# Performance work log

Hardware: AMD Instinct MI355X
Metric: run time of the kernel (lower is better)

Reference implementation:

```python
import jax, jax.numpy as jnp
import numpy as np

N_NODES = 100000
N_EDGES = 1600000
D_IN = 128
D_HID = 128
D_OUT = 32


def setup_inputs() -> dict:
    key = jax.random.key(0)
    ks = jax.random.split(key, 10)
    x = jax.random.normal(ks[0], (N_NODES, D_IN), dtype=jnp.float32)
    edge_index = jax.random.randint(ks[1], (2, N_EDGES), 0, N_NODES, dtype=jnp.int64)
    s = 0.05
    return {
        "x": x,
        "edge_index": edge_index,
        "Wl0": jax.random.normal(ks[2], (D_IN, D_HID), jnp.float32) * s,
        "bl0": jnp.zeros((D_HID,), jnp.float32),
        "Wr0": jax.random.normal(ks[3], (D_IN, D_HID), jnp.float32) * s,
        "Wl1": jax.random.normal(ks[4], (D_HID, D_HID), jnp.float32) * s,
        "bl1": jnp.zeros((D_HID,), jnp.float32),
        "Wr1": jax.random.normal(ks[5], (D_HID, D_HID), jnp.float32) * s,
        "Wl2": jax.random.normal(ks[6], (D_HID, D_OUT), jnp.float32) * s,
        "bl2": jnp.zeros((D_OUT,), jnp.float32),
        "Wr2": jax.random.normal(ks[7], (D_HID, D_OUT), jnp.float32) * s,
    }


def _sage_conv(x, src, dst, Wl, bl, Wr):
    # PyG SAGEConv (aggr='mean', root_weight=True):
    # out[i] = lin_l(mean_{j in N(i)} x_j) + lin_r(x_i)
    n = x.shape[0]
    msgs = x[src]                                        # [E, F] gather
    agg = jax.ops.segment_sum(msgs, dst, num_segments=n) # [N, F] scatter-add
    deg = jax.ops.segment_sum(jnp.ones((src.shape[0],), x.dtype), dst, num_segments=n)
    mean = agg / jnp.maximum(deg, 1.0)[:, None]
    return mean @ Wl + bl + x @ Wr


def reference(x, edge_index, Wl0, bl0, Wr0, Wl1, bl1, Wr1, Wl2, bl2, Wr2):
    src, dst = edge_index[0], edge_index[1]
    h = jax.nn.relu(_sage_conv(x, src, dst, Wl0, bl0, Wr0))
    h = jax.nn.relu(_sage_conv(h, src, dst, Wl1, bl1, Wr1))
    h = _sage_conv(h, src, dst, Wl2, bl2, Wr2)
    return jax.nn.log_softmax(h, axis=1)
```

## Files before the change

kernel.cpp:

```cpp
#include <hip/hip_runtime.h>
#include <hip/hip_bf16.h>
#include <math.h>

#define NN 100000
#define NE 1600000

#define NCB 391
#define EB  2048
#define SCT 512
#define EPT 4
#define HBK 128
#define NSB 782
#define WPB 144
#define NGB 782

typedef __attribute__((ext_vector_type(8))) short short8;
typedef __attribute__((ext_vector_type(4))) float f32x4;
typedef __attribute__((ext_vector_type(2))) float f32x2;

__device__ __forceinline__ unsigned short f2bf(float f) {
  union { float f; unsigned int i; } v; v.f = f;
  unsigned int i = v.i;
  unsigned int r = (i + 0x7FFFu + ((i >> 16) & 1u)) >> 16;
  return (unsigned short)r;
}
__device__ __forceinline__ float bflo(unsigned int u) {
  union { unsigned int i; float f; } v; v.i = u << 16; return v.f;
}
__device__ __forceinline__ float bfhi(unsigned int u) {
  union { unsigned int i; float f; } v; v.i = u & 0xFFFF0000u; return v.f;
}
__device__ __forceinline__ f32x2 up2(unsigned int u) {
  union { unsigned int i; float f; } lo, hi;
  lo.i = u << 16; hi.i = u & 0xFFFF0000u;
  return (f32x2){lo.f, hi.f};
}

__global__ __launch_bounds__(512) void k_prep(
    const int* __restrict__ dst, int* __restrict__ part,
    const float* __restrict__ Wl0, const float* __restrict__ Wr0,
    const float* __restrict__ Wl1, const float* __restrict__ Wr1,
    const float* __restrict__ Wl2, const float* __restrict__ Wr2,
    unsigned short* __restrict__ B0, unsigned short* __restrict__ B1,
    unsigned short* __restrict__ B2) {
  if (blockIdx.x < HBK) {
    __shared__ int h[NCB];
    for (int i = threadIdx.x; i < NCB; i += 512) h[i] = 0;
    __syncthreads();
    int stride = HBK * 512;
    for (int e = blockIdx.x * 512 + threadIdx.x; e < NE; e += stride) {
      int d = dst[e];
      d = d < 0 ? 0 : (d >= NN ? NN - 1 : d);
      atomicAdd(&h[d >> 8], 1);
    }
    __syncthreads();
    for (int i = threadIdx.x; i < NCB; i += 512) part[blockIdx.x * NCB + i] = h[i];
  } else {
    int idx = (blockIdx.x - HBK) * 512 + threadIdx.x;
    if (idx < 32768) {
      int n = idx >> 7, k = idx & 127;
      float v = (n < 128) ? Wl0[k * 128 + n] : Wr0[k * 128 + (n - 128)];
      B0[idx] = f2bf(v);
    } else if (idx < 65536) {
      int j = idx - 32768;
      int n = j >> 7, k = j & 127;
      float v = (n < 128) ? Wl1[k * 128 + n] : Wr1[k * 128 + (n - 128)];
      B1[j] = f2bf(v);
    } else if (idx < 73728) {
      int j = idx - 65536;
      int n = j >> 7, k = j & 127;
      float v = (n < 32) ? Wl2[k * 32 + n] : Wr2[k * 32 + (n - 32)];
      B2[j] = f2bf(v);
    }
  }
}

__global__ __launch_bounds__(512) void k_cscan(const int* __restrict__ part,
                                               int* __restrict__ cboff,
                                               int* __restrict__ ccur,
                                               int* __restrict__ csroff) {
  __shared__ int sd[512];
  int t = threadIdx.x;
  int v = 0;
  if (t < NCB) {
    int s0 = 0, s1 = 0, s2 = 0, s3 = 0;
    #pragma unroll 4
    for (int k = 0; k < HBK; k += 4) {
      s0 += part[(k + 0) * NCB + t];
      s1 += part[(k + 1) * NCB + t];
      s2 += part[(k + 2) * NCB + t];
      s3 += part[(k + 3) * NCB + t];
    }
    v = (s0 + s1) + (s2 + s3);
    ccur[t * 16] = 0;
  }
  sd[t] = v;
  __syncthreads();
  for (int st = 1; st < 512; st <<= 1) {
    int x = (t >= st) ? sd[t - st] : 0;
    __syncthreads();
    sd[t] += x;
    __syncthreads();
  }
  if (t < NCB) cboff[t] = sd[t] - v;
  if (t == NCB - 1) { cboff[NCB] = sd[t]; csroff[NN] = sd[t]; }
}


__device__ __forceinline__ void cscatter_body(
    char* smem, int bid,
    const int* __restrict__ src, const int* __restrict__ dst,
    const int* __restrict__ cboff, int* __restrict__ ccur,
    unsigned int* __restrict__ ebuf) {
  int* lh = (int*)smem;
  int t = threadIdx.x;
  int base = bid * EB;
  for (int i = t; i < NCB; i += SCT) lh[i] = 0;
  __syncthreads();
  unsigned int rk[EPT], pv[EPT];
  #pragma unroll
  for (int i = 0; i < EPT; i++) {
    int e = base + i * SCT + t;
    rk[i] = 0xFFFFFFFFu;
    pv[i] = 0;
    if (e < NE) {
      int d = dst[e];
      d = d < 0 ? 0 : (d >= NN ? NN - 1 : d);
      int s = src[e];
      s = s < 0 ? 0 : (s >= NN ? NN - 1 : s);
      int cb = d >> 8;
      int r = atomicAdd(&lh[cb], 1);
      rk[i] = (((unsigned int)cb) << 13) | (unsigned int)r;
      pv[i] = (((unsigned int)(d & 255)) << 17) | (unsigned int)s;
    }
  }
  __syncthreads();
  for (int i = t; i < NCB; i += SCT) {
    int c = lh[i];
    int g = c ? atomicAdd(&ccur[i * 16], c) : 0;
    lh[i] = cboff[i] + g;
  }
  __syncthreads();
  #pragma unroll
  for (int i = 0; i < EPT; i++) {
    unsigned int r = rk[i];
    if (r != 0xFFFFFFFFu) {
      ebuf[lh[r >> 13] + (r & 0x1FFF)] = pv[i];
    }
  }
}

__device__ __forceinline__ void epilogue256(
    unsigned short* sA, int tid, int nb, int wn, int mbase, int nbase,
    int l15, int lq, f32x4 acc[4][4], const float* __restrict__ bias,
    unsigned short* __restrict__ yl, unsigned short* __restrict__ yr) {
  __syncthreads();
  if (wn < 2) {
    #pragma unroll
    for (int mi = 0; mi < 4; mi++)
      #pragma unroll
      for (int ni = 0; ni < 4; ni++) {
        int n = nbase + ni * 16 + l15;
        #pragma unroll
        for (int r = 0; r < 4; r++)
          sA[(mbase + mi * 16 + lq * 4 + r) * 136 + n] = f2bf(acc[mi][ni][r]);
      }
  }
  __syncthreads();
  {
    int row = tid >> 2, c0 = (tid & 3) * 32;
    int gn = nb + row;
    if (gn < NN) {
      #pragma unroll
      for (int k = 0; k < 4; k++) {
        uint4 v = *(uint4*)&sA[row * 136 + c0 + k * 8];
        *(uint4*)&yl[(size_t)gn * 128 + c0 + k * 8] = v;
      }
    }
  }
  __syncthreads();
  if (wn >= 2) {
    #pragma unroll
    for (int mi = 0; mi < 4; mi++)
      #pragma unroll
      for (int ni = 0; ni < 4; ni++) {
        int n2 = nbase - 128 + ni * 16 + l15;
        float b = bias[n2];
        #pragma unroll
        for (int r = 0; r < 4; r++)
          sA[(mbase + mi * 16 + lq * 4 + r) * 136 + n2] =
              f2bf(acc[mi][ni][r] + b);
      }
  }
  __syncthreads();
  {
    int row = tid >> 2, c0 = (tid & 3) * 32;
    int gn = nb + row;
    if (gn < NN) {
      #pragma unroll
      for (int k = 0; k < 4; k++) {
        uint4 v = *(uint4*)&sA[row * 136 + c0 + k * 8];
        *(uint4*)&yr[(size_t)gn * 128 + c0 + k * 8] = v;
      }
    }
  }
}

__device__ __forceinline__ void mgemm0_body(
    char* smem, int bid, const float* __restrict__ A,
    const unsigned short* __restrict__ Bp, const float* __restrict__ bias,
    unsigned short* __restrict__ yl, unsigned short* __restrict__ yr) {
  unsigned short* sA = (unsigned short*)smem;
  int tid = threadIdx.x;
  int nb  = bid * 128;

  #pragma unroll
  for (int i = 0; i < 8; i++) {
    int j = i * 512 + tid;
    int m = j >> 5;
    int k4 = (j & 31) * 4;
    int gn = nb + m;
    float4 v = make_float4(0.f, 0.f, 0.f, 0.f);
    if (gn < NN) v = *(const float4*)&A[gn * 128 + k4];
    unsigned int p0 = (unsigned int)f2bf(v.x) | ((unsigned int)f2bf(v.y) << 16);
    unsigned int p1 = (unsigned int)f2bf(v.z) | ((unsigned int)f2bf(v.w) << 16);
    *(uint2*)&sA[m * 136 + k4] = make_uint2(p0, p1);
  }
  __syncthreads();

  int wave = tid >> 6, lane = tid & 63;
  int l15 = lane & 15, lq = lane >> 4;
  int wm = wave & 1, wn = wave >> 1;
  int mbase = wm * 64;
  int nbase = wn * 64;

  f32x4 acc[4][4];
  #pragma unroll
  for (int mi = 0; mi < 4; mi++)
    #pragma unroll
    for (int ni = 0; ni < 4; ni++) acc[mi][ni] = (f32x4){0.f, 0.f, 0.f, 0.f};

  #pragma unroll
  for (int kc = 0; kc < 4; kc++) {
    int k0 = kc * 32 + lq * 8;
    short8 af[4], bfr[4];
    #pragma unroll
    for (int ni = 0; ni < 4; ni++)
      bfr[ni] = *(const short8*)&Bp[(nbase + ni * 16 + l15) * 128 + k0];
    #pragma unroll
    for (int mi = 0; mi < 4; mi++)
      af[mi] = *(const short8*)&sA[(mbase + mi * 16 + l15) * 136 + k0];
    #pragma unroll
    for (int mi = 0; mi < 4; mi++)
      #pragma unroll
      for (int ni = 0; ni < 4; ni++)
        acc[mi][ni] = __builtin_amdgcn_mfma_f32_16x16x32_bf16(
            af[mi], bfr[ni], acc[mi][ni], 0, 0, 0);
  }

  epilogue256(sA, tid, nb, wn, mbase, nbase, l15, lq, acc, bias, yl, yr);
}

__global__ __launch_bounds__(512, 4) void k_scatgemm(
    const int* __restrict__ src, const int* __restrict__ dst,
    const int* __restrict__ cboff, int* __restrict__ ccur,
    unsigned int* __restrict__ ebuf,
    const float* __restrict__ x, const unsigned short* __restrict__ B0,
    const float* __restrict__ bias,
    unsigned short* __restrict__ yl, unsigned short* __restrict__ yr) {
  __shared__ char smem[128 * 136 * 2];
  int bid = blockIdx.x;
  if ((bid & 1) == 0) {
    cscatter_body(smem, bid >> 1, src, dst, cboff, ccur, ebuf);
  } else {
    mgemm0_body(smem, bid >> 1, x, B0, bias, yl, yr);
  }
}

__global__ __launch_bounds__(512) void k_crefine(
    const unsigned int* __restrict__ ebuf, const int* __restrict__ cboff,
    int* __restrict__ csroff, float* __restrict__ invd,
    int* __restrict__ csrsrc) {
  __shared__ int lh[256], pos[256], cur[256];
  int b = blockIdx.x, t = threadIdx.x;
  if (t < 256) { lh[t] = 0; cur[t] = 0; }
  __syncthreads();
  int beg = cboff[b], end = cboff[b + 1];
  for (int i = beg + t; i < end; i += 512) atomicAdd(&lh[ebuf[i] >> 17], 1);
  __syncthreads();
  int v = 0;
  if (t < 256) { v = lh[t]; pos[t] = v; }
  __syncthreads();
  for (int st = 1; st < 256; st <<= 1) {
    int x = (t < 256 && t >= st) ? pos[t - st] : 0;
    __syncthreads();
    if (t < 256) pos[t] += x;
    __syncthreads();
  }
  if (t < 256) {
    int nid = b * 256 + t;
    int mybase = cboff[b] + pos[t] - v;
    if (nid < NN) {
      csroff[nid] = mybase;
      invd[nid] = 1.0f / (float)(v < 1 ? 1 : v);
    }
    pos[t] = mybase;
  }
  __syncthreads();
  for (int i = beg + t; i < end; i += 512) {
    unsigned int u = ebuf[i];
    int local = u >> 17;
    int r = atomicAdd(&cur[local], 1);
    csrsrc[pos[local] + r] = (int)(u & 0x1FFFFu);
  }
}

template <int NC>
__global__ __launch_bounds__(512) void k_mgemm(
    const unsigned short* __restrict__ A, const unsigned short* __restrict__ Bp,
    const float* __restrict__ bias,
    unsigned short* __restrict__ yl, unsigned short* __restrict__ yr) {
  __shared__ unsigned short sA[128 * 136];
  int tid = threadIdx.x;
  int nb  = blockIdx.x * 128;

  #pragma unroll
  for (int i = 0; i < 4; i++) {
    int j = i * 512 + tid;
    int m = j >> 4;
    int k8 = (j & 15) * 8;
    int gn = nb + m;
    uint4 v = make_uint4(0, 0, 0, 0);
    if (gn < NN) v = *(const uint4*)&A[gn * 128 + k8];
    *(uint4*)&sA[m * 136 + k8] = v;
  }
  __syncthreads();

  int wave = tid >> 6, lane = tid & 63;
  int l15 = lane & 15, lq = lane >> 4;
  constexpr int MT = (NC == 256) ? 4 : 2;
  constexpr int NT = (NC == 256) ? 4 : 2;
  int wm, wn;
  if (NC == 256) { wm = wave & 1; wn = wave >> 1; }
  else           { wm = wave >> 1; wn = wave & 1; }
  int mbase = wm * (MT * 16);
  int nbase = wn * (NT * 16);

  f32x4 acc[MT][NT];
  #pragma unroll
  for (int mi = 0; mi < MT; mi++)
    #pragma unroll
    for (int ni = 0; ni < NT; ni++) acc[mi][ni] = (f32x4){0.f, 0.f, 0.f, 0.f};

  #pragma unroll
  for (int kc = 0; kc < 4; kc++) {
    int k0 = kc * 32 + lq * 8;
    short8 af[MT], bfr[NT];
    #pragma unroll
    for (int ni = 0; ni < NT; ni++)
      bfr[ni] = *(const short8*)&Bp[(nbase + ni * 16 + l15) * 128 + k0];
    #pragma unroll
    for (int mi = 0; mi < MT; mi++)
      af[mi] = *(const short8*)&sA[(mbase + mi * 16 + l15) * 136 + k0];
    #pragma unroll
    for (int mi = 0; mi < MT; mi++)
      #pragma unroll
      for (int ni = 0; ni < NT; ni++)
        acc[mi][ni] = __builtin_amdgcn_mfma_f32_16x16x32_bf16(
            af[mi], bfr[ni], acc[mi][ni], 0, 0, 0);
  }

  if (NC == 256) {
    f32x4 (*a)[4] = (f32x4(*)[4])acc;
    epilogue256(sA, tid, nb, wn, mbase, nbase, l15, lq, a, bias, yl, yr);
  } else {
    __syncthreads();
    #pragma unroll
    for (int mi = 0; mi < MT; mi++)
      #pragma unroll
      for (int ni = 0; ni < NT; ni++) {
        int n = nbase + ni * 16 + l15;
        float b = (n >= 32) ? bias[n - 32] : 0.f;
        #pragma unroll
        for (int r = 0; r < 4; r++)
          sA[(mbase + mi * 16 + lq * 4 + r) * 72 + n] =
              f2bf(acc[mi][ni][r] + b);
      }
    __syncthreads();
    int row = tid >> 2, c0 = (tid & 3) * 16;
    int gn = nb + row;
    if (gn < NN) {
      uint4 v0 = *(uint4*)&sA[row * 72 + c0];
      uint4 v1 = *(uint4*)&sA[row * 72 + c0 + 8];
      if (c0 < 32) {
        *(uint4*)&yl[(size_t)gn * 32 + c0] = v0;
        *(uint4*)&yl[(size_t)gn * 32 + c0 + 8] = v1;
      } else {
        *(uint4*)&yr[(size_t)gn * 32 + (c0 - 32)] = v0;
        *(uint4*)&yr[(size_t)gn * 32 + (c0 - 32) + 8] = v1;
      }
    }
  }
}

#define ACC8(u) do { \
  A01 += up2((u).x); A23 += up2((u).y); \
  A45 += up2((u).z); A67 += up2((u).w); } while (0)

__global__ __launch_bounds__(256) void k_agg128(
    const unsigned short* __restrict__ yl, const unsigned short* __restrict__ yr,
    const int* __restrict__ off, const int* __restrict__ csr,
    const float* __restrict__ invd, unsigned short* __restrict__ out, int relu) {
  int wid  = (blockIdx.x * 256 + threadIdx.x) >> 6;
  int lane = threadIdx.x & 63;
  if (wid >= NN) return;
  int beg = off[wid], end = off[wid + 1];
  int deg = end - beg;
  int q   = lane >> 4;
  int l16 = lane & 15;
  const uint4* ylp = (const uint4*)yl;

  float sc = invd[wid];
  uint4 rv = ((const uint4*)yr)[wid * 16 + l16];

  f32x2 A01 = (f32x2){0.f, 0.f}, A23 = (f32x2){0.f, 0.f};
  f32x2 A45 = (f32x2){0.f, 0.f}, A67 = (f32x2){0.f, 0.f};

  for (int w0 = 0; w0 < deg; w0 += 64) {
    int ei = w0 + lane;
    int sv = (ei < deg) ? csr[beg + ei] : 0;
    int wcnt = deg - w0; if (wcnt > 64) wcnt = 64;
    int full = wcnt >> 2;
    int p = 0;
    for (; p + 4 <= full; p += 4) {
      int b = p * 4 + q;
      int s0 = __shfl(sv, b,      64);
      int s1 = __shfl(sv, b + 4,  64);
      int s2 = __shfl(sv, b + 8,  64);
      int s3 = __shfl(sv, b + 12, 64);
      uint4 u0 = ylp[s0 * 16 + l16];
      uint4 u1 = ylp[s1 * 16 + l16];
      uint4 u2 = ylp[s2 * 16 + l16];
      uint4 u3 = ylp[s3 * 16 + l16];
      ACC8(u0); ACC8(u1); ACC8(u2); ACC8(u3);
    }
    for (; p < full; p++) {
      int s0 = __shfl(sv, p * 4 + q, 64);
      uint4 u0 = ylp[s0 * 16 + l16];
      ACC8(u0);
    }
    int rem = wcnt & 3;
    if (rem && q < rem) {
      int s0 = __shfl(sv, full * 4 + q, 64);
      uint4 u0 = ylp[s0 * 16 + l16];
      ACC8(u0);
    }
  }

  float a0 = A01.x, a1 = A01.y, a2 = A23.x, a3 = A23.y;
  float a4 = A45.x, a5 = A45.y, a6 = A67.x, a7 = A67.y;

  a0 += __shfl_xor(a0, 16, 64); a0 += __shfl_xor(a0, 32, 64);
  a1 += __shfl_xor(a1, 16, 64); a1 += __shfl_xor(a1, 32, 64);
  a2 += __shfl_xor(a2, 16, 64); a2 += __shfl_xor(a2, 32, 64);
  a3 += __shfl_xor(a3, 16, 64); a3 += __shfl_xor(a3, 32, 64);
  a4 += __shfl_xor(a4, 16, 64); a4 += __shfl_xor(a4, 32, 64);
  a5 += __shfl_xor(a5, 16, 64); a5 += __shfl_xor(a5, 32, 64);
  a6 += __shfl_xor(a6, 16, 64); a6 += __shfl_xor(a6, 32, 64);
  a7 += __shfl_xor(a7, 16, 64); a7 += __shfl_xor(a7, 32, 64);

  float v0 = a0 * sc + bflo(rv.x), v1 = a1 * sc + bfhi(rv.x);
  float v2 = a2 * sc + bflo(rv.y), v3 = a3 * sc + bfhi(rv.y);
  float v4 = a4 * sc + bflo(rv.z), v5 = a5 * sc + bfhi(rv.z);
  float v6 = a6 * sc + bflo(rv.w), v7 = a7 * sc + bfhi(rv.w);
  if (relu) {
    v0 = fmaxf(v0, 0.f); v1 = fmaxf(v1, 0.f);
    v2 = fmaxf(v2, 0.f); v3 = fmaxf(v3, 0.f);
    v4 = fmaxf(v4, 0.f); v5 = fmaxf(v5, 0.f);
    v6 = fmaxf(v6, 0.f); v7 = fmaxf(v7, 0.f);
  }
  if (q == 0) {
    unsigned int p0 = (unsigned int)f2bf(v0) | ((unsigned int)f2bf(v1) << 16);
    unsigned int p1 = (unsigned int)f2bf(v2) | ((unsigned int)f2bf(v3) << 16);
    unsigned int p2 = (unsigned int)f2bf(v4) | ((unsigned int)f2bf(v5) << 16);
    unsigned int p3 = (unsigned int)f2bf(v6) | ((unsigned int)f2bf(v7) << 16);
    ((uint4*)out)[wid * 16 + l16] = make_uint4(p0, p1, p2, p3);
  }
}

#define ACC4(u) do { \
  A01 += up2((u).x); A23 += up2((u).y); } while (0)

__global__ __launch_bounds__(256) void k_agg32_lsm(
    const unsigned short* __restrict__ yl, const unsigned short* __restrict__ yr,
    const int* __restrict__ off, const int* __restrict__ csr,
    const float* __restrict__ invd, float* __restrict__ out) {
  int wid  = (blockIdx.x * 256 + threadIdx.x) >> 6;
  int lane = threadIdx.x & 63;
  if (wid >= NN) return;
  int beg = off[wid], end = off[wid + 1];
  int deg = end - beg;
  int q  = lane >> 3;
  int l8 = lane & 7;
  const uint2* ylp = (const uint2*)yl;

  float sc = invd[wid];
  uint2 rv = ((const uint2*)yr)[wid * 8 + l8];

  f32x2 A01 = (f32x2){0.f, 0.f}, A23 = (f32x2){0.f, 0.f};

  for (int w0 = 0; w0 < deg; w0 += 64) {
    int ei = w0 + lane;
    int sv = (ei < deg) ? csr[beg + ei] : 0;
    int wcnt = deg - w0; if (wcnt > 64) wcnt = 64;
    int full = wcnt >> 3;
    int p = 0;
    for (; p + 2 <= full; p += 2) {
      int b = p * 8 + q;
      int s0 = __shfl(sv, b,     64);
      int s1 = __shfl(sv, b + 8, 64);
      uint2 u0 = ylp[s0 * 8 + l8];
      uint2 u1 = ylp[s1 * 8 + l8];
      ACC4(u0); ACC4(u1);
    }
    for (; p < full; p++) {
      int s0 = __shfl(sv, p * 8 + q, 64);
      uint2 u0 = ylp[s0 * 8 + l8];
      ACC4(u0);
    }
    int rem = wcnt & 7;
    if (rem && q < rem) {
      int s0 = __shfl(sv, full * 8 + q, 64);
      uint2 u0 = ylp[s0 * 8 + l8];
      ACC4(u0);
    }
  }

  float a0 = A01.x, a1 = A01.y, a2 = A23.x, a3 = A23.y;

  a0 += __shfl_xor(a0, 8, 64); a0 += __shfl_xor(a0, 16, 64); a0 += __shfl_xor(a0, 32, 64);
  a1 += __shfl_xor(a1, 8, 64); a1 += __shfl_xor(a1, 16, 64); a1 += __shfl_xor(a1, 32, 64);
  a2 += __shfl_xor(a2, 8, 64); a2 += __shfl_xor(a2, 16, 64); a2 += __shfl_xor(a2, 32, 64);
  a3 += __shfl_xor(a3, 8, 64); a3 += __shfl_xor(a3, 16, 64); a3 += __shfl_xor(a3, 32, 64);

  float v0 = a0 * sc + bflo(rv.x), v1 = a1 * sc + bfhi(rv.x);
  float v2 = a2 * sc + bflo(rv.y), v3 = a3 * sc + bfhi(rv.y);

  float m = fmaxf(fmaxf(v0, v1), fmaxf(v2, v3));
  m = fmaxf(m, __shfl_xor(m, 1, 64));
  m = fmaxf(m, __shfl_xor(m, 2, 64));
  m = fmaxf(m, __shfl_xor(m, 4, 64));
  float e0 = expf(v0 - m), e1 = expf(v1 - m);
  float e2 = expf(v2 - m), e3 = expf(v3 - m);
  float s = (e0 + e1) + (e2 + e3);
  s += __shfl_xor(s, 1, 64);
  s += __shfl_xor(s, 2, 64);
  s += __shfl_xor(s, 4, 64);
  float ls = logf(s);
  if (q == 0) {
    float4 o = make_float4(v0 - m - ls, v1 - m - ls, v2 - m - ls, v3 - m - ls);
    ((float4*)out)[wid * 8 + l8] = o;
  }
}


extern "C" void kernel_launch(void* const* d_in, const int* in_sizes, int n_in,
                              void* d_out, int out_size, void* d_ws, size_t ws_size,
                              hipStream_t stream) {
  (void)in_sizes; (void)n_in; (void)out_size; (void)ws_size;
  const float* x   = (const float*)d_in[0];
  const int*   ei  = (const int*)d_in[1];
  const float* Wl0 = (const float*)d_in[2];
  const float* bl0 = (const float*)d_in[3];
  const float* Wr0 = (const float*)d_in[4];
  const float* Wl1 = (const float*)d_in[5];
  const float* bl1 = (const float*)d_in[6];
  const float* Wr1 = (const float*)d_in[7];
  const float* Wl2 = (const float*)d_in[8];
  const float* bl2 = (const float*)d_in[9];
  const float* Wr2 = (const float*)d_in[10];
  const int* srcI = ei;
  const int* dstI = ei + NE;

  char* w = (char*)d_ws;
  int*   cboff  = (int*)(w + (32 << 10));
  unsigned short* B0 = (unsigned short*)(w + (64 << 10));
  unsigned short* B1 = (unsigned short*)(w + (160 << 10));
  unsigned short* B2 = (unsigned short*)(w + (256 << 10));
  int*   part   = (int*)(w + (288 << 10));
  int*   ccur   = (int*)(w + (496 << 10));
  int*   csroff = (int*)(w + (1024 << 10));
  float* invd   = (float*)(w + (1536 << 10));
  unsigned int* ebuf = (unsigned int*)(w + (size_t)(2) * 1024 * 1024);
  int*   csrsrc = (int*)(w + (size_t)(9) * 1024 * 1024);
  unsigned short* ylb = (unsigned short*)(w + (size_t)(16) * 1024 * 1024);
  unsigned short* yrb = (unsigned short*)(w + (size_t)(48) * 1024 * 1024);
  unsigned short* hb  = (unsigned short*)(w + (size_t)(80) * 1024 * 1024);

  dim3 gg(NGB);

  k_prep<<<HBK + WPB, 512, 0, stream>>>(dstI, part, Wl0, Wr0, Wl1, Wr1, Wl2, Wr2,
                                        B0, B1, B2);
  k_cscan<<<1, 512, 0, stream>>>(part, cboff, ccur, csroff);
  k_scatgemm<<<NSB + NGB, 512, 0, stream>>>(srcI, dstI, cboff, ccur, ebuf,
                                            x, B0, bl0, ylb, yrb);
  k_crefine<<<NCB, 512, 0, stream>>>(ebuf, cboff, csroff, invd, csrsrc);
  k_agg128<<<(NN * 64) / 256, 256, 0, stream>>>(ylb, yrb, csroff, csrsrc, invd, hb, 1);
  k_mgemm<256><<<gg, 512, 0, stream>>>(hb, B1, bl1, ylb, yrb);
  k_agg128<<<(NN * 64) / 256, 256, 0, stream>>>(ylb, yrb, csroff, csrsrc, invd, hb, 1);
  k_mgemm<64><<<gg, 512, 0, stream>>>(hb, B2, bl2, ylb, yrb);
  k_agg32_lsm<<<(NN * 64) / 256, 256, 0, stream>>>(ylb, yrb, csroff, csrsrc, invd,
                                                   (float*)d_out);
}
```

Baseline: 414.5 us.

## Overlap second-half aggregation with first-half GEMM in fused kernels

Splits each hidden layer's aggregation into two node halves. The first half runs alone. A fused kernel then interleaves GEMM blocks for the first half with aggregation waves for the second half, and a final GEMM launch covers the remaining rows. Layer outputs go to separate yl buffers so the fused kernel never overwrites inputs still being read. The scatter stage also doubles edges per block and changes the interleave ratio to 1 scatter block per 2 GEMM blocks. The split path is gated on workspace size, adds extra launches and relies on correct buffer aliasing.

```diff
diff --git a/kernel.cpp b/kernel.cpp
--- a/kernel.cpp
+++ b/kernel.cpp
@@ -6,13 +6,15 @@
 #define NE 1600000
 
 #define NCB 391
-#define EB  2048
+#define EB  4096
 #define SCT 512
-#define EPT 4
+#define EPT 8
 #define HBK 128
-#define NSB 782
+#define NSB 391
 #define WPB 144
 #define NGB 782
+#define HGB 391
+#define HNN 50048
 
 typedef __attribute__((ext_vector_type(8))) short short8;
 typedef __attribute__((ext_vector_type(4))) float f32x4;
@@ -106,7 +108,6 @@
   if (t == NCB - 1) { cboff[NCB] = sd[t]; csroff[NN] = sd[t]; }
 }
 
-
 __device__ __forceinline__ void cscatter_body(
     char* smem, int bid,
     const int* __restrict__ src, const int* __restrict__ dst,
@@ -258,7 +259,8 @@
             af[mi], bfr[ni], acc[mi][ni], 0, 0, 0);
   }
 
-  epilogue256(sA, tid, nb, wn, mbase, nbase, l15, lq, acc, bias, yl, yr);
+  epilogue256((unsigned short*)smem, tid, nb, wn, mbase, nbase, l15, lq, acc,
+              bias, yl, yr);
 }
 
 __global__ __launch_bounds__(512, 4) void k_scatgemm(
@@ -270,10 +272,11 @@
     unsigned short* __restrict__ yl, unsigned short* __restrict__ yr) {
   __shared__ char smem[128 * 136 * 2];
   int bid = blockIdx.x;
-  if ((bid & 1) == 0) {
-    cscatter_body(smem, bid >> 1, src, dst, cboff, ccur, ebuf);
+  int third = bid / 3;
+  if (bid - third * 3 == 0) {
+    cscatter_body(smem, third, src, dst, cboff, ccur, ebuf);
   } else {
-    mgemm0_body(smem, bid >> 1, x, B0, bias, yl, yr);
+    mgemm0_body(smem, bid - third - 1, x, B0, bias, yl, yr);
   }
 }
 
@@ -316,14 +319,11 @@
 }
 
 template <int NC>
-__global__ __launch_bounds__(512) void k_mgemm(
-    const unsigned short* __restrict__ A, const unsigned short* __restrict__ Bp,
-    const float* __restrict__ bias,
+__device__ __forceinline__ void mgemmN_body(
+    unsigned short* sA, int nb, const unsigned short* __restrict__ A,
+    const unsigned short* __restrict__ Bp, const float* __restrict__ bias,
     unsigned short* __restrict__ yl, unsigned short* __restrict__ yr) {
-  __shared__ unsigned short sA[128 * 136];
   int tid = threadIdx.x;
-  int nb  = blockIdx.x * 128;
-
   #pragma unroll
   for (int i = 0; i < 4; i++) {
     int j = i * 512 + tid;
@@ -403,17 +403,24 @@
   }
 }
 
+template <int NC>
+__global__ __launch_bounds__(512) void k_mgemm(
+    const unsigned short* __restrict__ A, const unsigned short* __restrict__ Bp,
+    const float* __restrict__ bias,
+    unsigned short* __restrict__ yl, unsigned short* __restrict__ yr, int gb) {
+  __shared__ unsigned short sA[128 * 136];
+  mgemmN_body<NC>(sA, (blockIdx.x + gb) * 128, A, Bp, bias, yl, yr);
+}
+
 #define ACC8(u) do { \
   A01 += up2((u).x); A23 += up2((u).y); \
   A45 += up2((u).z); A67 += up2((u).w); } while (0)
 
-__global__ __launch_bounds__(256) void k_agg128(
-    const unsigned short* __restrict__ yl, const unsigned short* __restrict__ yr,
-    const int* __restrict__ off, const int* __restrict__ csr,
-    const float* __restrict__ invd, unsigned short* __restrict__ out, int relu) {
-  int wid  = (blockIdx.x * 256 + threadIdx.x) >> 6;
-  int lane = threadIdx.x & 63;
-  if (wid >= NN) return;
+__device__ __forceinline__ void agg128_wave(
+    int wid, int lane, const unsigned short* __restrict__ yl,
+    const unsigned short* __restrict__ yr, const int* __restrict__ off,
+    const int* __restrict__ csr, const float* __restrict__ invd,
+    unsigned short* __restrict__ out) {
   int beg = off[wid], end = off[wid + 1];
   int deg = end - beg;
   int q   = lane >> 4;
@@ -469,22 +476,50 @@
   a6 += __shfl_xor(a6, 16, 64); a6 += __shfl_xor(a6, 32, 64);
   a7 += __shfl_xor(a7, 16, 64); a7 += __shfl_xor(a7, 32, 64);
 
-  float v0 = a0 * sc + bflo(rv.x), v1 = a1 * sc + bfhi(rv.x);
-  float v2 = a2 * sc + bflo(rv.y), v3 = a3 * sc + bfhi(rv.y);
-  float v4 = a4 * sc + bflo(rv.z), v5 = a5 * sc + bfhi(rv.z);
-  float v6 = a6 * sc + bflo(rv.w), v7 = a7 * sc + bfhi(rv.w);
-  if (relu) {
-    v0 = fmaxf(v0, 0.f); v1 = fmaxf(v1, 0.f);
-    v2 = fmaxf(v2, 0.f); v3 = fmaxf(v3, 0.f);
-    v4 = fmaxf(v4, 0.f); v5 = fmaxf(v5, 0.f);
-    v6 = fmaxf(v6, 0.f); v7 = fmaxf(v7, 0.f);
-  }
+  float v0 = fmaxf(a0 * sc + bflo(rv.x), 0.f);
+  float v1 = fmaxf(a1 * sc + bfhi(rv.x), 0.f);
+  float v2 = fmaxf(a2 * sc + bflo(rv.y), 0.f);
+  float v3 = fmaxf(a3 * sc + bfhi(rv.y), 0.f);
+  float v4 = fmaxf(a4 * sc + bflo(rv.z), 0.f);
+  float v5 = fmaxf(a5 * sc + bfhi(rv.z), 0.f);
+  float v6 = fmaxf(a6 * sc + bflo(rv.w), 0.f);
+  float v7 = fmaxf(a7 * sc + bfhi(rv.w), 0.f);
   if (q == 0) {
     unsigned int p0 = (unsigned int)f2bf(v0) | ((unsigned int)f2bf(v1) << 16);
     unsigned int p1 = (unsigned int)f2bf(v2) | ((unsigned int)f2bf(v3) << 16);
     unsigned int p2 = (unsigned int)f2bf(v4) | ((unsigned int)f2bf(v5) << 16);
     unsigned int p3 = (unsigned int)f2bf(v6) | ((unsigned int)f2bf(v7) << 16);
     ((uint4*)out)[wid * 16 + l16] = make_uint4(p0, p1, p2, p3);
+  }
+}
+
+__global__ __launch_bounds__(256) void k_agg128(
+    const unsigned short* __restrict__ yl, const unsigned short* __restrict__ yr,
+    const int* __restrict__ off, const int* __restrict__ csr,
+    const float* __restrict__ invd, unsigned short* __restrict__ out,
+    int base, int lim) {
+  int wid = base + ((blockIdx.x * 256 + threadIdx.x) >> 6);
+  if (wid >= lim) return;
+  agg128_wave(wid, threadIdx.x & 63, yl, yr, off, csr, invd, out);
+}
+
+template <int NC>
+__global__ __launch_bounds__(512, 4) void k_agggemm(
+    const unsigned short* __restrict__ ylin, const unsigned short* __restrict__ yrin,
+    const int* __restrict__ off, const int* __restrict__ csr,
+    const float* __restrict__ invd, unsigned short* __restrict__ hb,
+    const unsigned short* __restrict__ Bp, const float* __restrict__ bias,
+    unsigned short* __restrict__ outl, unsigned short* __restrict__ outr) {
+  __shared__ unsigned short sA[128 * 136];
+  int bid = blockIdx.x;
+  int g = bid / 17;
+  if (bid - g * 17 == 0) {
+    mgemmN_body<NC>(sA, g * 128, hb, Bp, bias, outl, outr);
+  } else {
+    int idx = bid - g - 1;
+    int wid = HNN + idx * 8 + (threadIdx.x >> 6);
+    if (wid < NN)
+      agg128_wave(wid, threadIdx.x & 63, ylin, yrin, off, csr, invd, hb);
   }
 }
 
@@ -567,7 +602,7 @@
 extern "C" void kernel_launch(void* const* d_in, const int* in_sizes, int n_in,
                               void* d_out, int out_size, void* d_ws, size_t ws_size,
                               hipStream_t stream) {
-  (void)in_sizes; (void)n_in; (void)out_size; (void)ws_size;
+  (void)in_sizes; (void)n_in; (void)out_size;
   const float* x   = (const float*)d_in[0];
   const int*   ei  = (const int*)d_in[1];
   const float* Wl0 = (const float*)d_in[2];
@@ -593,22 +628,41 @@
   float* invd   = (float*)(w + (1536 << 10));
   unsigned int* ebuf = (unsigned int*)(w + (size_t)(2) * 1024 * 1024);
   int*   csrsrc = (int*)(w + (size_t)(9) * 1024 * 1024);
-  unsigned short* ylb = (unsigned short*)(w + (size_t)(16) * 1024 * 1024);
-  unsigned short* yrb = (unsigned short*)(w + (size_t)(48) * 1024 * 1024);
+  unsigned short* yl0 = (unsigned short*)(w + (size_t)(16) * 1024 * 1024);
+  unsigned short* yr0 = (unsigned short*)(w + (size_t)(48) * 1024 * 1024);
   unsigned short* hb  = (unsigned short*)(w + (size_t)(80) * 1024 * 1024);
-
-  dim3 gg(NGB);
+  unsigned short* yl1 = (unsigned short*)(w + (size_t)(112) * 1024 * 1024);
+  unsigned short* yl2 = (unsigned short*)(w + (size_t)(16) * 1024 * 1024);
+  unsigned short* yr2 = (unsigned short*)(w + (size_t)(26) * 1024 * 1024);
 
   k_prep<<<HBK + WPB, 512, 0, stream>>>(dstI, part, Wl0, Wr0, Wl1, Wr1, Wl2, Wr2,
                                         B0, B1, B2);
   k_cscan<<<1, 512, 0, stream>>>(part, cboff, ccur, csroff);
   k_scatgemm<<<NSB + NGB, 512, 0, stream>>>(srcI, dstI, cboff, ccur, ebuf,
-                                            x, B0, bl0, ylb, yrb);
+                                            x, B0, bl0, yl0, yr0);
   k_crefine<<<NCB, 512, 0, stream>>>(ebuf, cboff, csroff, invd, csrsrc);
-  k_agg128<<<(NN * 64) / 256, 256, 0, stream>>>(ylb, yrb, csroff, csrsrc, invd, hb, 1);
-  k_mgemm<256><<<gg, 512, 0, stream>>>(hb, B1, bl1, ylb, yrb);
-  k_agg128<<<(NN * 64) / 256, 256, 0, stream>>>(ylb, yrb, csroff, csrsrc, invd, hb, 1);
-  k_mgemm<64><<<gg, 512, 0, stream>>>(hb, B2, bl2, ylb, yrb);
-  k_agg32_lsm<<<(NN * 64) / 256, 256, 0, stream>>>(ylb, yrb, csroff, csrsrc, invd,
-                                                   (float*)d_out);
-}
+
+  if (ws_size >= ((size_t)144 << 20)) {
+    k_agg128<<<HNN / 4, 256, 0, stream>>>(yl0, yr0, csroff, csrsrc, invd, hb,
+                                          0, HNN);
+    k_agggemm<256><<<6635, 512, 0, stream>>>(yl0, yr0, csroff, csrsrc, invd,
+                                             hb, B1, bl1, yl1, yr0);
+    k_mgemm<256><<<HGB, 512, 0, stream>>>(hb, B1, bl1, yl1, yr0, HGB);
+    k_agg128<<<HNN / 4, 256, 0, stream>>>(yl1, yr0, csroff, csrsrc, invd, hb,
+                                          0, HNN);
+    k_agggemm<64><<<6635, 512, 0, stream>>>(yl1, yr0, csroff, csrsrc, invd,
+                                            hb, B2, bl2, yl2, yr2);
+    k_mgemm<64><<<HGB, 512, 0, stream>>>(hb, B2, bl2, yl2, yr2, HGB);
+    k_agg32_lsm<<<(NN * 64) / 256, 256, 0, stream>>>(yl2, yr2, csroff, csrsrc,
+                                                     invd, (float*)d_out);
+  } else {
+    k_agg128<<<(NN * 64) / 256, 256, 0, stream>>>(yl0, yr0, csroff, csrsrc,
+                                                  invd, hb, 0, NN);
+    k_mgemm<256><<<NGB, 512, 0, stream>>>(hb, B1, bl1, yl0, yr0, 0);
+    k_agg128<<<(NN * 64) / 256, 256, 0, stream>>>(yl0, yr0, csroff, csrsrc,
+                                                  invd, hb, 0, NN);
+    k_mgemm<64><<<NGB, 512, 0, stream>>>(hb, B2, bl2, yl2, yr2, 0);
+    k_agg32_lsm<<<(NN * 64) / 256, 256, 0, stream>>>(yl2, yr2, csroff, csrsrc,
+                                                     invd, (float*)d_out);
+  }
+}
```

Result: no change. 412.0 us (-0.6%).
